# Performance work log

Measured on AMD Instinct MI355X. Metric: run time of the kernel, lower is better.

Reference implementation:

```python
import jax, jax.numpy as jnp
import numpy as np

EPS = 1e-12
BETA = 3.0
N_TH = 21


def setup_inputs() -> dict:
    key = jax.random.key(0)
    k1, k2 = jax.random.split(key)
    N, C = 65536, 1000
    logits = jax.random.normal(k1, (N, C), dtype=jnp.float32)
    labels = jax.random.randint(k2, (N,), 0, C, dtype=jnp.int64)
    idx = jnp.arange(N, dtype=jnp.int64)
    return {"logits": logits, "labels": labels, "idx": idx, "type": 0}


def _forward(logits, labels):
    # probs / confidences / predictions
    probs = jax.nn.softmax(logits, axis=1)                      # [N, C]
    conf = jnp.max(probs, axis=1)                               # [N]
    preds = jnp.argmax(probs, axis=1)                           # [N]
    # predictive uncertainty (type == 0): entropy of softmax
    unc = -jnp.sum(probs * jnp.log(probs + EPS), axis=-1)       # [N]
    umin, umax = jnp.min(unc), jnp.max(unc)
    th = jnp.linspace(0.0, 1.0, N_TH, dtype=logits.dtype)       # [21]
    unc_th = umin + th * (umax - umin)                          # [21]

    acc = (labels == preds)                                     # [N] bool
    t_unc = jnp.tanh(unc)                                       # [N]
    certain = unc[None, :] <= unc_th[:, None]                   # [21, N]
    a = acc[None, :]

    zero = jnp.zeros((), logits.dtype)
    n_ac = jnp.sum(jnp.where(a & certain, conf * (1.0 - t_unc), zero), axis=1)
    n_au = jnp.sum(jnp.where(a & ~certain, conf * t_unc, zero), axis=1)
    n_ic = jnp.sum(jnp.where(~a & certain, (1.0 - conf) * (1.0 - t_unc), zero), axis=1)
    n_iu = jnp.sum(jnp.where(~a & ~certain, (1.0 - conf) * t_unc, zero), axis=1)

    avu = (n_ac + n_iu) / (n_ac + n_au + n_ic + n_iu + EPS)     # [21]
    # sklearn.metrics.auc == trapezoidal rule over (th, avu)
    auc_avu = 0.5 * jnp.sum((avu[1:] + avu[:-1]) * (th[1:] - th[:-1]))
    # original wraps auc in a fresh tensor -> no grad through the AvU branch
    avu_loss = -BETA * jnp.log(jax.lax.stop_gradient(auc_avu) + EPS)

    logp = jax.nn.log_softmax(logits, axis=1)                   # [N, C]
    ce = -jnp.mean(jnp.take_along_axis(logp, labels[:, None], axis=1))
    return (avu_loss + ce)[None]                                # [1], matches torch


def reference(logits, labels, idx, type) -> jnp.ndarray:
    del idx, type  # idx unused; type=0 path (predictive uncertainty)
    return _forward(logits, labels)
```

## Files before the change

### kernel.cpp

```cpp
#include <hip/hip_runtime.h>
#include <math.h>

#define NROWS 65536
#define NC    1000
#define NTH   21
#define NBLK1 4096

__device__ __forceinline__ void amax2(float va, int ia, float vb, int ib,
                                      float& vo, int& io) {
    bool t = (va >= vb);
    vo = t ? va : vb;
    io = t ? ia : ib;
}

__device__ __forceinline__ void row_process(
        float4 r0, float4 r1, float4 r2, float4 r3,
        int lane, int label, int row,
        float* __restrict__ unc_o, float* __restrict__ confs_o,
        float& mn, float& mx, float& ssum)
{
    int b0 = lane << 2, b1 = (lane + 64) << 2, b2 = (lane + 128) << 2, b3 = (lane + 192) << 2;
    float mA, mB, mC, mD, mt0, mt1, m; int iA, iB, iC, iD, it0, it1, mi;
    {
        float p, q; int pi, qi;
        amax2(r0.x, b0+0, r0.y, b0+1, p, pi); amax2(r0.z, b0+2, r0.w, b0+3, q, qi);
        amax2(p, pi, q, qi, mA, iA);
        amax2(r1.x, b1+0, r1.y, b1+1, p, pi); amax2(r1.z, b1+2, r1.w, b1+3, q, qi);
        amax2(p, pi, q, qi, mB, iB);
        amax2(r2.x, b2+0, r2.y, b2+1, p, pi); amax2(r2.z, b2+2, r2.w, b2+3, q, qi);
        amax2(p, pi, q, qi, mC, iC);
        amax2(r3.x, b3+0, r3.y, b3+1, p, pi); amax2(r3.z, b3+2, r3.w, b3+3, q, qi);
        amax2(p, pi, q, qi, mD, iD);
    }
    amax2(mA, iA, mB, iB, mt0, it0);
    amax2(mC, iC, mD, iD, mt1, it1);
    amax2(mt0, it0, mt1, it1, m, mi);

    #pragma unroll
    for (int off = 1; off < 64; off <<= 1) {
        float om = __shfl_xor(m, off, 64);
        int   oi = __shfl_xor(mi, off, 64);
        if (om > m || (om == m && oi < mi)) { m = om; mi = oi; }
    }

    float se = 0.f, sx = 0.f;
#define ACCUM(v) { float t_ = (v) - m; float e_ = __expf(t_); se += e_; sx = fmaf(e_, t_, sx); }
    ACCUM(r0.x) ACCUM(r0.y) ACCUM(r0.z) ACCUM(r0.w)
    ACCUM(r1.x) ACCUM(r1.y) ACCUM(r1.z) ACCUM(r1.w)
    ACCUM(r2.x) ACCUM(r2.y) ACCUM(r2.z) ACCUM(r2.w)
    ACCUM(r3.x) ACCUM(r3.y) ACCUM(r3.z) ACCUM(r3.w)
#undef ACCUM
    #pragma unroll
    for (int off = 1; off < 64; off <<= 1) {
        se += __shfl_xor(se, off, 64);
        sx += __shfl_xor(sx, off, 64);
    }

    float Z    = se;
    float logZ = logf(Z);
    float conf = 1.0f / Z;
    float uncv = logZ - sx / Z;

    int f4 = label >> 2, slot = label & 3, it = f4 >> 6;
    float4 q = (it == 0) ? r0 : (it == 1) ? r1 : (it == 2) ? r2 : r3;
    float cand = (slot == 0) ? q.x : (slot == 1) ? q.y : (slot == 2) ? q.z : q.w;
    float xl = __shfl(cand, f4 & 63, 64);
    float lp = (xl - m) - logZ;

    if (lane == 0) {
        unc_o[row]   = uncv;
        confs_o[row] = (mi == label) ? conf : -conf;
    }
    mn = fminf(mn, uncv);
    mx = fmaxf(mx, uncv);
    ssum += lp;
}

#define LOADROW(P, q0, q1, q2, q3) \
    q0 = (P)[lane]; q1 = (P)[lane + 64]; q2 = (P)[lane + 128]; \
    q3 = make_float4(-1e30f, -1e30f, -1e30f, -1e30f); \
    if (lane < 58) q3 = (P)[lane + 192];

__global__ __launch_bounds__(256, 4) void k1_rowstats(
        const float* __restrict__ logits, const int* __restrict__ labels,
        float* __restrict__ unc_o, float* __restrict__ confs_o,
        float* __restrict__ blk_mn, float* __restrict__ blk_mx, float* __restrict__ blk_s)
{
    const int wave = threadIdx.x >> 6;
    const int lane = threadIdx.x & 63;
    const int row0 = (blockIdx.x * 4 + wave) * 4;
    const float4* p = (const float4*)(logits + (size_t)row0 * NC);

    int lab0 = labels[row0], lab1 = labels[row0 + 1];
    int lab2 = labels[row0 + 2], lab3 = labels[row0 + 3];

    float mn = 1e30f, mx = -1e30f, ssum = 0.f;
    float4 a0, a1, a2, a3, b0, b1, b2, b3;

    LOADROW(p,        a0, a1, a2, a3)
    LOADROW(p + 250,  b0, b1, b2, b3)
    row_process(a0, a1, a2, a3, lane, lab0, row0,     unc_o, confs_o, mn, mx, ssum);
    LOADROW(p + 500,  a0, a1, a2, a3)
    row_process(b0, b1, b2, b3, lane, lab1, row0 + 1, unc_o, confs_o, mn, mx, ssum);
    LOADROW(p + 750,  b0, b1, b2, b3)
    row_process(a0, a1, a2, a3, lane, lab2, row0 + 2, unc_o, confs_o, mn, mx, ssum);
    row_process(b0, b1, b2, b3, lane, lab3, row0 + 3, unc_o, confs_o, mn, mx, ssum);

    __shared__ float s_mn[4], s_mx[4], s_s[4];
    if (lane == 0) { s_mn[wave] = mn; s_mx[wave] = mx; s_s[wave] = ssum; }
    __syncthreads();
    if (threadIdx.x == 0) {
        blk_mn[blockIdx.x] = fminf(fminf(s_mn[0], s_mn[1]), fminf(s_mn[2], s_mn[3]));
        blk_mx[blockIdx.x] = fmaxf(fmaxf(s_mx[0], s_mx[1]), fmaxf(s_mx[2], s_mx[3]));
        blk_s [blockIdx.x] = (s_s[0] + s_s[1]) + (s_s[2] + s_s[3]);
    }
}

__global__ __launch_bounds__(256) void k2_reduce(
        const float* __restrict__ blk_mn, const float* __restrict__ blk_mx,
        const float* __restrict__ blk_s,
        float* __restrict__ ce_sum, unsigned* __restrict__ umin_b,
        unsigned* __restrict__ umax_b, float* __restrict__ bins)
{
    float mn = 1e30f, mx = -1e30f, s = 0.f;
    for (int i = threadIdx.x; i < NBLK1; i += 256) {
        mn = fminf(mn, blk_mn[i]);
        mx = fmaxf(mx, blk_mx[i]);
        s += blk_s[i];
    }
    #pragma unroll
    for (int off = 1; off < 64; off <<= 1) {
        mn = fminf(mn, __shfl_xor(mn, off, 64));
        mx = fmaxf(mx, __shfl_xor(mx, off, 64));
        s += __shfl_xor(s, off, 64);
    }
    __shared__ float smn[4], smx[4], ss[4];
    int wave = threadIdx.x >> 6;
    if ((threadIdx.x & 63) == 0) { smn[wave] = mn; smx[wave] = mx; ss[wave] = s; }
    __syncthreads();
    if (threadIdx.x == 0) {
        mn = fminf(fminf(smn[0], smn[1]), fminf(smn[2], smn[3]));
        mx = fmaxf(fmaxf(smx[0], smx[1]), fmaxf(smx[2], smx[3]));
        s  = (ss[0] + ss[1]) + (ss[2] + ss[3]);
        *ce_sum = s;
        *umin_b = __float_as_uint(mn);
        *umax_b = __float_as_uint(mx);
    }
    if (threadIdx.x < 88) bins[threadIdx.x] = 0.f;
}

__global__ __launch_bounds__(256) void k3_hist(
        const float* __restrict__ unc, const float* __restrict__ confs,
        const unsigned* __restrict__ umin_b, const unsigned* __restrict__ umax_b,
        float* __restrict__ bins)
{
    __shared__ float h[88];
    for (int i = threadIdx.x; i < 88; i += 256) h[i] = 0.f;
    __syncthreads();
    float umin = __uint_as_float(*umin_b);
    float umax = __uint_as_float(*umax_b);
    float du = umax - umin;

    int i = blockIdx.x * 256 + threadIdx.x;
    float u  = unc[i];
    float cs = confs[i];
    float conf = fabsf(cs);
    bool  acc  = cs > 0.f;
    float tu = tanhf(u);

    int b = NTH;
    #pragma unroll
    for (int t = NTH - 1; t >= 0; --t) {
        float th = umin + ((float)t * 0.05f) * du;
        if (u <= th) b = t;
    }
    float w = acc ? conf : (1.f - conf);
    int base = acc ? 0 : 44;
    atomicAdd(&h[base + b],       w * (1.f - tu));
    atomicAdd(&h[base + 22 + b],  w * tu);
    __syncthreads();
    for (int i2 = threadIdx.x; i2 < 88; i2 += 256) {
        float v = h[i2];
        if (v != 0.f) atomicAdd(&bins[i2], v);
    }
}

__global__ void k4_final(const float* __restrict__ bins, const float* __restrict__ ce_sum,
                         float* __restrict__ out)
{
    if (threadIdx.x != 0 || blockIdx.x != 0) return;
    float tot_au = 0.f, tot_iu = 0.f;
    for (int b = 0; b < 22; ++b) { tot_au += bins[22 + b]; tot_iu += bins[66 + b]; }
    float cac = 0.f, cau = 0.f, cic = 0.f, ciu = 0.f;
    float avu[NTH];
    for (int t = 0; t < NTH; ++t) {
        cac += bins[t]; cau += bins[22 + t]; cic += bins[44 + t]; ciu += bins[66 + t];
        float nac = cac, nau = tot_au - cau, nic = cic, niu = tot_iu - ciu;
        avu[t] = (nac + niu) / (nac + nau + nic + niu + 1e-12f);
    }
    float auc = 0.f;
    for (int t = 0; t + 1 < NTH; ++t) auc += 0.5f * (avu[t + 1] + avu[t]) * 0.05f;
    float avu_loss = -3.0f * logf(auc + 1e-12f);
    float ce = -(*ce_sum) / (float)NROWS;
    out[0] = avu_loss + ce;
}

extern "C" void kernel_launch(void* const* d_in, const int* in_sizes, int n_in,
                              void* d_out, int out_size, void* d_ws, size_t ws_size,
                              hipStream_t stream)
{
    const float* logits = (const float*)d_in[0];
    const int*   labels = (const int*)d_in[1];
    float* ws    = (float*)d_ws;
    float* unc   = ws;
    float* confs = ws + NROWS;
    float* bins  = ws + 2 * NROWS;
    float* ce_sum = ws + 2 * NROWS + 1024;
    unsigned* umin_b = (unsigned*)(ws + 2 * NROWS + 2048);
    unsigned* umax_b = (unsigned*)(ws + 2 * NROWS + 3072);
    float* blk_mn = ws + 2 * NROWS + 4096;
    float* blk_mx = blk_mn + NBLK1;
    float* blk_s  = blk_mx + NBLK1;

    hipLaunchKernelGGL(k1_rowstats, dim3(NBLK1), dim3(256), 0, stream,
                       logits, labels, unc, confs, blk_mn, blk_mx, blk_s);
    hipLaunchKernelGGL(k2_reduce, dim3(1), dim3(256), 0, stream,
                       blk_mn, blk_mx, blk_s, ce_sum, umin_b, umax_b, bins);
    hipLaunchKernelGGL(k3_hist, dim3(NROWS / 256), dim3(256), 0, stream,
                       unc, confs, umin_b, umax_b, bins);
    hipLaunchKernelGGL(k4_final, dim3(1), dim3(64), 0, stream,
                       bins, ce_sum, (float*)d_out);
}
```

Baseline: 371.9 us.

## Fuse global reduce into histogram kernel and process eight rows per wave

The single-block reduction kernel is removed. Each histogram block now redundantly reduces the per-block min, max and CE partials itself, and the bins are zeroed inside the row-stats kernel. The row-stats kernel also handles eight rows per wave instead of four, which halves the block count and the partial-array size that each histogram block has to re-reduce. This saves one kernel launch and a serial single-block step. In exchange, every histogram block rereads 2048 partials, and the longer per-wave loop may lower memory-level parallelism in the 262 MB read pass.

```diff
diff --git a/kernel.cpp b/kernel.cpp
--- a/kernel.cpp
+++ b/kernel.cpp
@@ -4,7 +4,7 @@
 #define NROWS 65536
 #define NC    1000
 #define NTH   21
-#define NBLK1 4096
+#define NBLK1 2048
 
 __device__ __forceinline__ void amax2(float va, int ia, float vb, int ib,
                                       float& vo, int& io) {
@@ -84,27 +84,40 @@
 __global__ __launch_bounds__(256, 4) void k1_rowstats(
         const float* __restrict__ logits, const int* __restrict__ labels,
         float* __restrict__ unc_o, float* __restrict__ confs_o,
-        float* __restrict__ blk_mn, float* __restrict__ blk_mx, float* __restrict__ blk_s)
-{
+        float* __restrict__ blk_mn, float* __restrict__ blk_mx, float* __restrict__ blk_s,
+        float* __restrict__ bins)
+{
+    if (blockIdx.x == 0 && threadIdx.x < 88) bins[threadIdx.x] = 0.f;
+
     const int wave = threadIdx.x >> 6;
     const int lane = threadIdx.x & 63;
-    const int row0 = (blockIdx.x * 4 + wave) * 4;
+    const int row0 = (blockIdx.x * 4 + wave) * 8;
     const float4* p = (const float4*)(logits + (size_t)row0 * NC);
 
-    int lab0 = labels[row0], lab1 = labels[row0 + 1];
+    int lab0 = labels[row0],     lab1 = labels[row0 + 1];
     int lab2 = labels[row0 + 2], lab3 = labels[row0 + 3];
+    int lab4 = labels[row0 + 4], lab5 = labels[row0 + 5];
+    int lab6 = labels[row0 + 6], lab7 = labels[row0 + 7];
 
     float mn = 1e30f, mx = -1e30f, ssum = 0.f;
     float4 a0, a1, a2, a3, b0, b1, b2, b3;
 
-    LOADROW(p,        a0, a1, a2, a3)
-    LOADROW(p + 250,  b0, b1, b2, b3)
+    LOADROW(p,         a0, a1, a2, a3)
+    LOADROW(p + 250,   b0, b1, b2, b3)
     row_process(a0, a1, a2, a3, lane, lab0, row0,     unc_o, confs_o, mn, mx, ssum);
-    LOADROW(p + 500,  a0, a1, a2, a3)
+    LOADROW(p + 500,   a0, a1, a2, a3)
     row_process(b0, b1, b2, b3, lane, lab1, row0 + 1, unc_o, confs_o, mn, mx, ssum);
-    LOADROW(p + 750,  b0, b1, b2, b3)
+    LOADROW(p + 750,   b0, b1, b2, b3)
     row_process(a0, a1, a2, a3, lane, lab2, row0 + 2, unc_o, confs_o, mn, mx, ssum);
+    LOADROW(p + 1000,  a0, a1, a2, a3)
     row_process(b0, b1, b2, b3, lane, lab3, row0 + 3, unc_o, confs_o, mn, mx, ssum);
+    LOADROW(p + 1250,  b0, b1, b2, b3)
+    row_process(a0, a1, a2, a3, lane, lab4, row0 + 4, unc_o, confs_o, mn, mx, ssum);
+    LOADROW(p + 1500,  a0, a1, a2, a3)
+    row_process(b0, b1, b2, b3, lane, lab5, row0 + 5, unc_o, confs_o, mn, mx, ssum);
+    LOADROW(p + 1750,  b0, b1, b2, b3)
+    row_process(a0, a1, a2, a3, lane, lab6, row0 + 6, unc_o, confs_o, mn, mx, ssum);
+    row_process(b0, b1, b2, b3, lane, lab7, row0 + 7, unc_o, confs_o, mn, mx, ssum);
 
     __shared__ float s_mn[4], s_mx[4], s_s[4];
     if (lane == 0) { s_mn[wave] = mn; s_mx[wave] = mx; s_s[wave] = ssum; }
@@ -116,12 +129,16 @@
     }
 }
 
-__global__ __launch_bounds__(256) void k2_reduce(
+__global__ __launch_bounds__(256) void k23_hist(
         const float* __restrict__ blk_mn, const float* __restrict__ blk_mx,
         const float* __restrict__ blk_s,
-        float* __restrict__ ce_sum, unsigned* __restrict__ umin_b,
-        unsigned* __restrict__ umax_b, float* __restrict__ bins)
-{
+        const float* __restrict__ unc, const float* __restrict__ confs,
+        float* __restrict__ ce_sum, float* __restrict__ bins)
+{
+    __shared__ float h[88];
+    __shared__ float smn[4], smx[4], ss[4];
+    for (int i = threadIdx.x; i < 88; i += 256) h[i] = 0.f;
+
     float mn = 1e30f, mx = -1e30f, s = 0.f;
     for (int i = threadIdx.x; i < NBLK1; i += 256) {
         mn = fminf(mn, blk_mn[i]);
@@ -134,31 +151,20 @@
         mx = fmaxf(mx, __shfl_xor(mx, off, 64));
         s += __shfl_xor(s, off, 64);
     }
-    __shared__ float smn[4], smx[4], ss[4];
     int wave = threadIdx.x >> 6;
     if ((threadIdx.x & 63) == 0) { smn[wave] = mn; smx[wave] = mx; ss[wave] = s; }
     __syncthreads();
     if (threadIdx.x == 0) {
         mn = fminf(fminf(smn[0], smn[1]), fminf(smn[2], smn[3]));
         mx = fmaxf(fmaxf(smx[0], smx[1]), fmaxf(smx[2], smx[3]));
-        s  = (ss[0] + ss[1]) + (ss[2] + ss[3]);
-        *ce_sum = s;
-        *umin_b = __float_as_uint(mn);
-        *umax_b = __float_as_uint(mx);
-    }
-    if (threadIdx.x < 88) bins[threadIdx.x] = 0.f;
-}
-
-__global__ __launch_bounds__(256) void k3_hist(
-        const float* __restrict__ unc, const float* __restrict__ confs,
-        const unsigned* __restrict__ umin_b, const unsigned* __restrict__ umax_b,
-        float* __restrict__ bins)
-{
-    __shared__ float h[88];
-    for (int i = threadIdx.x; i < 88; i += 256) h[i] = 0.f;
-    __syncthreads();
-    float umin = __uint_as_float(*umin_b);
-    float umax = __uint_as_float(*umax_b);
+        smn[0] = mn; smx[0] = mx;
+        if (blockIdx.x == 0) {
+            *ce_sum = (ss[0] + ss[1]) + (ss[2] + ss[3]);
+        }
+    }
+    __syncthreads();
+    float umin = smn[0];
+    float umax = smx[0];
     float du = umax - umin;
 
     int i = blockIdx.x * 256 + threadIdx.x;
@@ -216,18 +222,14 @@
     float* confs = ws + NROWS;
     float* bins  = ws + 2 * NROWS;
     float* ce_sum = ws + 2 * NROWS + 1024;
-    unsigned* umin_b = (unsigned*)(ws + 2 * NROWS + 2048);
-    unsigned* umax_b = (unsigned*)(ws + 2 * NROWS + 3072);
     float* blk_mn = ws + 2 * NROWS + 4096;
     float* blk_mx = blk_mn + NBLK1;
     float* blk_s  = blk_mx + NBLK1;
 
     hipLaunchKernelGGL(k1_rowstats, dim3(NBLK1), dim3(256), 0, stream,
-                       logits, labels, unc, confs, blk_mn, blk_mx, blk_s);
-    hipLaunchKernelGGL(k2_reduce, dim3(1), dim3(256), 0, stream,
-                       blk_mn, blk_mx, blk_s, ce_sum, umin_b, umax_b, bins);
-    hipLaunchKernelGGL(k3_hist, dim3(NROWS / 256), dim3(256), 0, stream,
-                       unc, confs, umin_b, umax_b, bins);
+                       logits, labels, unc, confs, blk_mn, blk_mx, blk_s, bins);
+    hipLaunchKernelGGL(k23_hist, dim3(NROWS / 256), dim3(256), 0, stream,
+                       blk_mn, blk_mx, blk_s, unc, confs, ce_sum, bins);
     hipLaunchKernelGGL(k4_final, dim3(1), dim3(64), 0, stream,
                        bins, ce_sum, (float*)d_out);
 }
```

Result: no change. 377.4 us (+1.5%).
